# Performance work log

Hardware: AMD Instinct MI355X
Metric: run time of the kernel (lower is better)

Reference implementation:

```python
import jax, jax.numpy as jnp
import numpy as np


def setup_inputs() -> dict:
    key = jax.random.key(0)
    k1, k2 = jax.random.split(key)
    x = jax.random.normal(k1, (32, 512, 512, 1), dtype=jnp.float32)
    se = jnp.ones((3, 3), dtype=jnp.float32)
    rank = jax.random.normal(k2, (9,), dtype=jnp.float32)
    return {"x": x, "se": se, "rank": rank}


def _extract_patches_3x3_same(x):
    # x: [B, H, W, 1] -> [B, H, W, 9], zero-padded SAME, row-major window order
    B, H, W, C = x.shape
    xp = jnp.pad(x, ((0, 0), (1, 1), (1, 1), (0, 0)))
    shifts = [xp[:, dy:dy + H, dx:dx + W, 0] for dy in range(3) for dx in range(3)]
    return jnp.stack(shifts, axis=-1)  # [B, H, W, 9]


def reference(x, se, rank):
    # Faithful to Morph2D.call: patches * se, sort ascending over the 9-window,
    # softmax(rank)-weighted sum -> soft rank-order filter.
    patches = _extract_patches_3x3_same(x)              # [B,H,W,9]
    weighted = patches * se.reshape(9)                  # elementwise by SE
    sorted_p = jnp.sort(weighted, axis=-1)              # ascending over window
    w = jax.nn.softmax(rank)                            # [9]
    out = jnp.sum(sorted_p * w, axis=-1)                # [B,H,W]
    return out.reshape(x.shape)                         # [B,H,W,1]
```

## Files before the change

kernel.cpp:

```cpp
#include <hip/hip_runtime.h>


#define BB 32
#define HH 512
#define WW 512

#define CSWAP(a,b) { float lo_ = fminf(v[a], v[b]); float hi_ = fmaxf(v[a], v[b]); v[a] = lo_; v[b] = hi_; }

__global__ __launch_bounds__(256) void morph2d_kernel(
    const float* __restrict__ x, const float* __restrict__ se9,
    const float* __restrict__ rank, float* __restrict__ out)
{
    int nper = gridDim.x >> 3;
    int lb   = (blockIdx.x & 7) * nper + (blockIdx.x >> 3);
    int g    = lb * 256 + threadIdx.x;

    int gx = g & 127;
    int yg = (g >> 7) & 255;
    int b  = g >> 15;
    int x4 = gx << 2;
    int y0 = yg << 1;

    float se[9], w[9];
    {
        float r[9]; float m = -3.4e38f;
        #pragma unroll
        for (int i = 0; i < 9; ++i) { r[i] = rank[i]; m = fmaxf(m, r[i]); }
        float s = 0.f;
        #pragma unroll
        for (int i = 0; i < 9; ++i) { r[i] = __expf(r[i] - m); s += r[i]; }
        float inv = 1.0f / s;
        #pragma unroll
        for (int i = 0; i < 9; ++i) { w[i] = r[i] * inv; se[i] = se9[i]; }
    }

    const float* img = x + (size_t)b * (HH * WW);
    float rv[4][6];
    #pragma unroll
    for (int r = 0; r < 4; ++r) {
        int ry  = y0 - 1 + r;
        int ryc = min(max(ry, 0), HH - 1);
        const float* row = img + ryc * WW;
        float4 c  = *(const float4*)(row + x4);
        float  lf = row[max(x4 - 1, 0)];
        float  rt = row[min(x4 + 4, WW - 1)];
        float  m  = (ry >= 0 && ry < HH) ? 1.0f : 0.0f;
        rv[r][0] = ((x4 == 0)       ? 0.f : lf) * m;
        rv[r][1] = c.x * m;
        rv[r][2] = c.y * m;
        rv[r][3] = c.z * m;
        rv[r][4] = c.w * m;
        rv[r][5] = ((x4 + 4 >= WW)  ? 0.f : rt) * m;
    }

    #pragma unroll
    for (int r = 0; r < 2; ++r) {
        float4 res;
        float* resp = &res.x;
        #pragma unroll
        for (int j = 0; j < 4; ++j) {
            float v[9];
            #pragma unroll
            for (int dy = 0; dy < 3; ++dy) {
                v[dy*3+0] = rv[r+dy][j]   * se[dy*3+0];
                v[dy*3+1] = rv[r+dy][j+1] * se[dy*3+1];
                v[dy*3+2] = rv[r+dy][j+2] * se[dy*3+2];
            }
            CSWAP(0,3) CSWAP(1,7) CSWAP(2,5) CSWAP(4,8)
            CSWAP(0,7) CSWAP(2,4) CSWAP(3,8) CSWAP(5,6)
            CSWAP(0,2) CSWAP(1,3) CSWAP(4,5) CSWAP(7,8)
            CSWAP(1,4) CSWAP(3,6) CSWAP(5,7)
            CSWAP(0,1) CSWAP(2,4) CSWAP(3,5) CSWAP(6,8)
            CSWAP(2,3) CSWAP(4,5) CSWAP(6,7)
            CSWAP(1,2) CSWAP(3,4) CSWAP(5,6)

            float acc = 0.f;
            #pragma unroll
            for (int i = 0; i < 9; ++i) acc = fmaf(v[i], w[i], acc);
            resp[j] = acc;
        }
        *(float4*)(out + (((size_t)b * HH + (y0 + r)) * WW + x4)) = res;
    }
}

extern "C" void kernel_launch(void* const* d_in, const int* in_sizes, int n_in,
                              void* d_out, int out_size, void* d_ws, size_t ws_size,
                              hipStream_t stream) {
    const float* x    = (const float*)d_in[0];
    const float* se   = (const float*)d_in[1];
    const float* rank = (const float*)d_in[2];
    float* out = (float*)d_out;

    const int total_threads = BB * (HH / 2) * (WW / 4);
    morph2d_kernel<<<total_threads / 256, 256, 0, stream>>>(x, se, rank, out);
}
```

Before: 101.1 us.

## Process one output row per thread with fast interior path and scalarized weights

Each thread now produces one output row of four pixels instead of two rows, which doubles the thread count and raises the occupancy hint to 8 blocks per CU. Interior rows take a branch that skips the clamping and masking logic. The softmax drops max-subtraction and applies the normalization once after the weighted sum, and readfirstlane keeps weights and SE values in scalar registers. The cost is more redundant halo loads per output (3 rows per output row instead of 4 per 2), and skipping max-subtraction risks exp overflow for large rank values.

Result: faster. 96.58 us (-4.5%).

```diff
diff --git a/kernel.cpp b/kernel.cpp
--- a/kernel.cpp
+++ b/kernel.cpp
@@ -1,13 +1,13 @@
 #include <hip/hip_runtime.h>
 
 
-#define BB 32
 #define HH 512
 #define WW 512
 
+#define RFL(x) __int_as_float(__builtin_amdgcn_readfirstlane(__float_as_int(x)))
 #define CSWAP(a,b) { float lo_ = fminf(v[a], v[b]); float hi_ = fmaxf(v[a], v[b]); v[a] = lo_; v[b] = hi_; }
 
-__global__ __launch_bounds__(256) void morph2d_kernel(
+__global__ __launch_bounds__(256, 8) void morph2d_kernel(
     const float* __restrict__ x, const float* __restrict__ se9,
     const float* __restrict__ rank, float* __restrict__ out)
 {
@@ -16,71 +16,83 @@
     int g    = lb * 256 + threadIdx.x;
 
     int gx = g & 127;
-    int yg = (g >> 7) & 255;
-    int b  = g >> 15;
+    int y  = (g >> 7) & 511;
+    int b  = g >> 16;
     int x4 = gx << 2;
-    int y0 = yg << 1;
 
-    float se[9], w[9];
-    {
-        float r[9]; float m = -3.4e38f;
+    const float* img = x + (size_t)b * (HH * WW);
+    int offL = max(x4 - 1, 0);
+    int offR = min(x4 + 4, WW - 1);
+
+    float rv[3][6];
+    if (y > 0 && y < HH - 1) {
+        const float* p = img + (y - 1) * WW;
         #pragma unroll
-        for (int i = 0; i < 9; ++i) { r[i] = rank[i]; m = fmaxf(m, r[i]); }
-        float s = 0.f;
+        for (int r = 0; r < 3; ++r) {
+            float4 c = *(const float4*)(p + x4);
+            float lf = p[offL];
+            float rt = p[offR];
+            rv[r][0] = lf;  rv[r][1] = c.x; rv[r][2] = c.y;
+            rv[r][3] = c.z; rv[r][4] = c.w; rv[r][5] = rt;
+            p += WW;
+        }
+    } else {
         #pragma unroll
-        for (int i = 0; i < 9; ++i) { r[i] = __expf(r[i] - m); s += r[i]; }
-        float inv = 1.0f / s;
-        #pragma unroll
-        for (int i = 0; i < 9; ++i) { w[i] = r[i] * inv; se[i] = se9[i]; }
+        for (int r = 0; r < 3; ++r) {
+            int ry  = y - 1 + r;
+            int ryc = min(max(ry, 0), HH - 1);
+            const float* p = img + ryc * WW;
+            float  m = (ry >= 0 && ry < HH) ? 1.f : 0.f;
+            float4 c = *(const float4*)(p + x4);
+            rv[r][0] = p[offL] * m; rv[r][1] = c.x * m; rv[r][2] = c.y * m;
+            rv[r][3] = c.z * m;     rv[r][4] = c.w * m; rv[r][5] = p[offR] * m;
+        }
     }
 
-    const float* img = x + (size_t)b * (HH * WW);
-    float rv[4][6];
-    #pragma unroll
-    for (int r = 0; r < 4; ++r) {
-        int ry  = y0 - 1 + r;
-        int ryc = min(max(ry, 0), HH - 1);
-        const float* row = img + ryc * WW;
-        float4 c  = *(const float4*)(row + x4);
-        float  lf = row[max(x4 - 1, 0)];
-        float  rt = row[min(x4 + 4, WW - 1)];
-        float  m  = (ry >= 0 && ry < HH) ? 1.0f : 0.0f;
-        rv[r][0] = ((x4 == 0)       ? 0.f : lf) * m;
-        rv[r][1] = c.x * m;
-        rv[r][2] = c.y * m;
-        rv[r][3] = c.z * m;
-        rv[r][4] = c.w * m;
-        rv[r][5] = ((x4 + 4 >= WW)  ? 0.f : rt) * m;
+    float w[9], se[9];
+    float inv_s;
+    {
+        float s = 0.f;
+        float e[9];
+        #pragma unroll
+        for (int i = 0; i < 9; ++i) { e[i] = __expf(rank[i]); s += e[i]; }
+        inv_s = RFL(1.0f / s);
+        #pragma unroll
+        for (int i = 0; i < 9; ++i) { w[i] = RFL(e[i]); se[i] = RFL(se9[i]); }
     }
 
     #pragma unroll
-    for (int r = 0; r < 2; ++r) {
-        float4 res;
-        float* resp = &res.x;
+    for (int r = 0; r < 3; ++r) {
+        rv[r][0] = (x4 == 0)       ? 0.f : rv[r][0];
+        rv[r][5] = (x4 + 4 >= WW)  ? 0.f : rv[r][5];
+    }
+
+    float4 res;
+    float* resp = &res.x;
+    #pragma unroll
+    for (int j = 0; j < 4; ++j) {
+        float v[9];
         #pragma unroll
-        for (int j = 0; j < 4; ++j) {
-            float v[9];
-            #pragma unroll
-            for (int dy = 0; dy < 3; ++dy) {
-                v[dy*3+0] = rv[r+dy][j]   * se[dy*3+0];
-                v[dy*3+1] = rv[r+dy][j+1] * se[dy*3+1];
-                v[dy*3+2] = rv[r+dy][j+2] * se[dy*3+2];
-            }
-            CSWAP(0,3) CSWAP(1,7) CSWAP(2,5) CSWAP(4,8)
-            CSWAP(0,7) CSWAP(2,4) CSWAP(3,8) CSWAP(5,6)
-            CSWAP(0,2) CSWAP(1,3) CSWAP(4,5) CSWAP(7,8)
-            CSWAP(1,4) CSWAP(3,6) CSWAP(5,7)
-            CSWAP(0,1) CSWAP(2,4) CSWAP(3,5) CSWAP(6,8)
-            CSWAP(2,3) CSWAP(4,5) CSWAP(6,7)
-            CSWAP(1,2) CSWAP(3,4) CSWAP(5,6)
+        for (int dy = 0; dy < 3; ++dy) {
+            v[dy*3+0] = rv[dy][j]   * se[dy*3+0];
+            v[dy*3+1] = rv[dy][j+1] * se[dy*3+1];
+            v[dy*3+2] = rv[dy][j+2] * se[dy*3+2];
+        }
+        CSWAP(0,3) CSWAP(1,7) CSWAP(2,5) CSWAP(4,8)
+        CSWAP(0,7) CSWAP(2,4) CSWAP(3,8) CSWAP(5,6)
+        CSWAP(0,2) CSWAP(1,3) CSWAP(4,5) CSWAP(7,8)
+        CSWAP(1,4) CSWAP(3,6) CSWAP(5,7)
+        CSWAP(0,1) CSWAP(2,4) CSWAP(3,5) CSWAP(6,8)
+        CSWAP(2,3) CSWAP(4,5) CSWAP(6,7)
+        CSWAP(1,2) CSWAP(3,4) CSWAP(5,6)
 
-            float acc = 0.f;
-            #pragma unroll
-            for (int i = 0; i < 9; ++i) acc = fmaf(v[i], w[i], acc);
-            resp[j] = acc;
-        }
-        *(float4*)(out + (((size_t)b * HH + (y0 + r)) * WW + x4)) = res;
+        float acc = 0.f;
+        #pragma unroll
+        for (int i = 0; i < 9; ++i) acc = fmaf(v[i], w[i], acc);
+        resp[j] = acc * inv_s;
     }
+
+    *(float4*)(out + (((size_t)b * HH + y) * WW + x4)) = res;
 }
 
 extern "C" void kernel_launch(void* const* d_in, const int* in_sizes, int n_in,
@@ -91,6 +103,6 @@
     const float* rank = (const float*)d_in[2];
     float* out = (float*)d_out;
 
-    const int total_threads = BB * (HH / 2) * (WW / 4);
+    const int total_threads = 32 * HH * (WW / 4);
     morph2d_kernel<<<total_threads / 256, 256, 0, stream>>>(x, se, rank, out);
 }
```
